# Optimization experiments

Measured on AMD Instinct MI355X. Metric: run time of the kernel, lower is better.

## Reference

```python
import jax, jax.numpy as jnp
import numpy as np

N_NODES = 100000
N_EDGES = 1600000
IN_CH = 128
HID = 128   # 2 * out_channels
OUT = 64


def setup_inputs() -> dict:
    key = jax.random.key(0)
    ks = jax.random.split(key, 5)
    x = jax.random.normal(ks[0], (N_NODES, IN_CH), dtype=jnp.float32)
    edge_index = jax.random.randint(ks[1], (2, N_EDGES), 0, N_NODES, dtype=jnp.int64)
    # Glorot-ish init for the two GCN weight matrices
    W1 = jax.random.normal(ks[2], (IN_CH, HID), dtype=jnp.float32) / np.sqrt(IN_CH)
    b1 = jnp.zeros((HID,), dtype=jnp.float32)
    W2 = jax.random.normal(ks[3], (HID, OUT), dtype=jnp.float32) / np.sqrt(HID)
    b2 = jnp.zeros((OUT,), dtype=jnp.float32)
    return {"x": x, "edge_index": edge_index, "W1": W1, "b1": b1, "W2": W2, "b2": b2}


def _gcn_conv(x, W, b, src, dst, coef, n):
    # Standard GCNConv: D^{-1/2} (A + I) D^{-1/2} X W + b
    xw = x @ W                                   # [N, F_out]
    msg = xw[src] * coef[:, None]                # gather + scale  [E+N, F_out]
    agg = jax.ops.segment_sum(msg, dst, num_segments=n)  # scatter-add [N, F_out]
    return agg + b


def reference(x, edge_index, W1, b1, W2, b2):
    n = x.shape[0]
    loops = jnp.arange(n, dtype=edge_index.dtype)
    src = jnp.concatenate([edge_index[0], loops])  # add self loops
    dst = jnp.concatenate([edge_index[1], loops])
    deg = jax.ops.segment_sum(jnp.ones_like(src, dtype=x.dtype), dst, num_segments=n)
    dinv = jnp.where(deg > 0, jax.lax.rsqrt(deg), 0.0)
    coef = dinv[src] * dinv[dst]                  # symmetric normalization per edge

    h = _gcn_conv(x, W1, b1, src, dst, coef, n)
    h = jax.nn.relu(h)                            # non_linearity=True
    # F.normalize(p=2, dim=-1) with eps clamp 1e-12; dropout inactive (eval mode)
    h = h / jnp.maximum(jnp.linalg.norm(h, axis=-1, keepdims=True), 1e-12)
    return _gcn_conv(h, W2, b2, src, dst, coef, n)
```

## Files before the change

### kernel.cpp

```cpp
#include <hip/hip_runtime.h>
#include <hip/hip_bf16.h>


#define IN_CH 128
#define HID 128
#define OUT_CH 64
#define NBLK 128
#define MAXNB 1568

typedef unsigned int uint_t;
typedef unsigned short ushort_t;
typedef __attribute__((ext_vector_type(8))) short bf16x8;
typedef __attribute__((ext_vector_type(4))) float f32x4;
typedef __attribute__((ext_vector_type(2))) float f32v2;

__device__ __forceinline__ ushort_t f32_to_bf16_rn(float f) {
    uint_t u = __float_as_uint(f);
    u = (u + 0x7fffu + ((u >> 16) & 1u)) >> 16;
    return (ushort_t)u;
}
__device__ __forceinline__ float bf16lo_to_f32(uint_t u) { return __uint_as_float(u << 16); }
__device__ __forceinline__ float bf16hi_to_f32(uint_t u) { return __uint_as_float(u & 0xffff0000u); }

__device__ __forceinline__ void acc_row(f32v2& a0, f32v2& a1, f32v2& a2, f32v2& a3,
                                        uint4 v) {
    a0 += (f32v2){bf16lo_to_f32(v.x), bf16hi_to_f32(v.x)};
    a1 += (f32v2){bf16lo_to_f32(v.y), bf16hi_to_f32(v.y)};
    a2 += (f32v2){bf16lo_to_f32(v.z), bf16hi_to_f32(v.z)};
    a3 += (f32v2){bf16lo_to_f32(v.w), bf16hi_to_f32(v.w)};
}
__device__ __forceinline__ void acc_row_c(f32v2& a0, f32v2& a1, f32v2& a2, f32v2& a3,
                                          uint4 v, float c) {
    f32v2 cv = {c, c};
    a0 += (f32v2){bf16lo_to_f32(v.x), bf16hi_to_f32(v.x)} * cv;
    a1 += (f32v2){bf16lo_to_f32(v.y), bf16hi_to_f32(v.y)} * cv;
    a2 += (f32v2){bf16lo_to_f32(v.z), bf16hi_to_f32(v.z)} * cv;
    a3 += (f32v2){bf16lo_to_f32(v.w), bf16hi_to_f32(v.w)} * cv;
}

__global__ __launch_bounds__(256) void hist_kernel(const int* __restrict__ dst, int E,
                                                   int chunk, int NB,
                                                   int* __restrict__ blk_cnt) {
    __shared__ int hist[MAXNB];
    int tid = threadIdx.x;
    int blk = blockIdx.x;
    for (int b = tid; b < NB; b += 256) hist[b] = 0;
    __syncthreads();
    int start = blk * chunk;
    int end = start + chunk; if (end > E) end = E;
    int e = start + tid;
    for (; e + 768 < end; e += 1024) {
        int d0 = dst[e], d1 = dst[e + 256], d2 = dst[e + 512], d3 = dst[e + 768];
        atomicAdd(&hist[d0 >> 6], 1);
        atomicAdd(&hist[d1 >> 6], 1);
        atomicAdd(&hist[d2 >> 6], 1);
        atomicAdd(&hist[d3 >> 6], 1);
    }
    for (; e < end; e += 256) atomicAdd(&hist[dst[e] >> 6], 1);
    __syncthreads();
    for (int b = tid; b < NB; b += 256) blk_cnt[blk * NB + b] = hist[b];
}

__global__ __launch_bounds__(256) void btot_kernel(const int* __restrict__ blk_cnt,
                                                   int NB, int* __restrict__ btot) {
    int b = blockIdx.x * 256 + threadIdx.x;
    if (b < NB) {
        int sum = 0;
        #pragma unroll 8
        for (int blk = 0; blk < NBLK; blk++) sum += blk_cnt[blk * NB + b];
        btot[b] = sum;
    }
}

__global__ __launch_bounds__(256) void scan_kernel(const int* __restrict__ btot, int NB,
                                                   int* __restrict__ bucket_base,
                                                   int* __restrict__ row_start,
                                                   int n, int E) {
    __shared__ int sdata[256];
    __shared__ int carryS;
    int tid = threadIdx.x;
    if (tid == 0) carryS = 0;
    __syncthreads();
    int nchunks = (NB + 255) / 256;
    for (int c = 0; c < nchunks; c++) {
        int i = c * 256 + tid;
        int v = (i < NB) ? btot[i] : 0;
        sdata[tid] = v;
        __syncthreads();
        for (int off = 1; off < 256; off <<= 1) {
            int t = (tid >= off) ? sdata[tid - off] : 0;
            __syncthreads();
            sdata[tid] += t;
            __syncthreads();
        }
        if (i < NB) bucket_base[i] = carryS + sdata[tid] - v;
        __syncthreads();
        if (tid == 0) carryS += sdata[255];
        __syncthreads();
    }
    if (tid == 0) {
        bucket_base[NB] = E;
        row_start[n] = E;
    }
}

__global__ __launch_bounds__(256) void colscan_kernel(const int* __restrict__ blk_cnt,
                                                      const int* __restrict__ bucket_base,
                                                      int NB, int* __restrict__ blk_start) {
    __shared__ int tile[NBLK][16];
    int tid = threadIdx.x;
    int b0 = blockIdx.x * 16;
    for (int idx = tid; idx < NBLK * 16; idx += 256) {
        int blk = idx >> 4, b = idx & 15;
        if (b0 + b < NB) tile[blk][b] = blk_cnt[blk * NB + b0 + b];
    }
    __syncthreads();
    if (tid < 16 && b0 + tid < NB) {
        int running = bucket_base[b0 + tid];
        for (int blk = 0; blk < NBLK; blk++) {
            int t = tile[blk][tid];
            tile[blk][tid] = running;
            running += t;
        }
    }
    __syncthreads();
    for (int idx = tid; idx < NBLK * 16; idx += 256) {
        int blk = idx >> 4, b = idx & 15;
        if (b0 + b < NB) blk_start[blk * NB + b0 + b] = tile[blk][b];
    }
}

__global__ __launch_bounds__(256) void scatter_kernel(const int* __restrict__ src,
                                                      const int* __restrict__ dst,
                                                      int E, int chunk, int NB,
                                                      const int* __restrict__ blk_start,
                                                      uint_t* __restrict__ pairs) {
    __shared__ int cur[MAXNB];
    int tid = threadIdx.x;
    int blk = blockIdx.x;
    for (int b = tid; b < NB; b += 256) cur[b] = blk_start[blk * NB + b];
    __syncthreads();
    int start = blk * chunk;
    int end = start + chunk; if (end > E) end = E;
    int e = start + tid;
    for (; e + 768 < end; e += 1024) {
        int d0 = dst[e], d1 = dst[e + 256], d2 = dst[e + 512], d3 = dst[e + 768];
        int s0 = src[e], s1 = src[e + 256], s2 = src[e + 512], s3 = src[e + 768];
        int p0 = atomicAdd(&cur[d0 >> 6], 1);
        int p1 = atomicAdd(&cur[d1 >> 6], 1);
        int p2 = atomicAdd(&cur[d2 >> 6], 1);
        int p3 = atomicAdd(&cur[d3 >> 6], 1);
        pairs[p0] = (uint_t)s0 | ((uint_t)(d0 & 63) << 26);
        pairs[p1] = (uint_t)s1 | ((uint_t)(d1 & 63) << 26);
        pairs[p2] = (uint_t)s2 | ((uint_t)(d2 & 63) << 26);
        pairs[p3] = (uint_t)s3 | ((uint_t)(d3 & 63) << 26);
    }
    for (; e < end; e += 256) {
        int d = dst[e], s = src[e];
        int p = atomicAdd(&cur[d >> 6], 1);
        pairs[p] = (uint_t)s | ((uint_t)(d & 63) << 26);
    }
}

__global__ __launch_bounds__(256) void fine_fill_kernel(const uint_t* __restrict__ pairs,
                                                        const int* __restrict__ bucket_base,
                                                        int* __restrict__ row_start,
                                                        float* __restrict__ dinv,
                                                        int* __restrict__ csr_src,
                                                        int n) {
    __shared__ int cnt64[64];
    __shared__ int cur[64];
    int b = blockIdx.x;
    int node0 = b << 6;
    int tid = threadIdx.x;
    if (tid < 64) cnt64[tid] = 0;
    __syncthreads();
    int start = bucket_base[b];
    int end = bucket_base[b + 1];
    int e = start + tid;
    for (; e + 768 < end; e += 1024) {
        uint_t u0 = pairs[e], u1 = pairs[e + 256], u2 = pairs[e + 512], u3 = pairs[e + 768];
        atomicAdd(&cnt64[u0 >> 26], 1);
        atomicAdd(&cnt64[u1 >> 26], 1);
        atomicAdd(&cnt64[u2 >> 26], 1);
        atomicAdd(&cnt64[u3 >> 26], 1);
    }
    for (; e < end; e += 256) atomicAdd(&cnt64[pairs[e] >> 26], 1);
    __syncthreads();
    if (tid < 64) {
        int c = cnt64[tid];
        int v = c;
        #pragma unroll
        for (int off = 1; off < 64; off <<= 1) {
            int u = __shfl_up(v, off, 64);
            if (tid >= off) v += u;
        }
        int excl = start + v - c;
        if (node0 + tid < n) {
            row_start[node0 + tid] = excl;
            dinv[node0 + tid] = rsqrtf((float)(c + 1));
        }
        cur[tid] = excl;
    }
    __syncthreads();
    e = start + tid;
    for (; e + 768 < end; e += 1024) {
        uint_t u0 = pairs[e], u1 = pairs[e + 256], u2 = pairs[e + 512], u3 = pairs[e + 768];
        int p0 = atomicAdd(&cur[u0 >> 26], 1);
        int p1 = atomicAdd(&cur[u1 >> 26], 1);
        int p2 = atomicAdd(&cur[u2 >> 26], 1);
        int p3 = atomicAdd(&cur[u3 >> 26], 1);
        csr_src[p0] = (int)(u0 & 0x3FFFFFFu);
        csr_src[p1] = (int)(u1 & 0x3FFFFFFu);
        csr_src[p2] = (int)(u2 & 0x3FFFFFFu);
        csr_src[p3] = (int)(u3 & 0x3FFFFFFu);
    }
    for (; e < end; e += 256) {
        uint_t u = pairs[e];
        int p = atomicAdd(&cur[u >> 26], 1);
        csr_src[p] = (int)(u & 0x3FFFFFFu);
    }
}

__global__ __launch_bounds__(256) void wsplit_kernel(const float* __restrict__ W1,
                                                     const float* __restrict__ W2,
                                                     ushort_t* __restrict__ w1h,
                                                     ushort_t* __restrict__ w1l,
                                                     ushort_t* __restrict__ w2h,
                                                     ushort_t* __restrict__ w2l) {
    int idx = blockIdx.x * 256 + threadIdx.x;
    const int tot1 = 128 * 128;
    const int tot = tot1 + 64 * 128;
    if (idx >= tot) return;
    float v;
    ushort_t* ph;
    ushort_t* pl;
    int o;
    if (idx < tot1) {
        int c = idx >> 7, k = idx & 127;
        v = W1[k * 128 + c];
        ph = w1h; pl = w1l; o = idx;
    } else {
        int j = idx - tot1;
        int c = j >> 7, k = j & 127;
        v = W2[k * 64 + c];
        ph = w2h; pl = w2l; o = j;
    }
    ushort_t h = f32_to_bf16_rn(v);
    float hv = __uint_as_float((uint_t)h << 16);
    ph[o] = h;
    pl[o] = f32_to_bf16_rn(v - hv);
}

template <int NCOL, bool F32_IN>
__global__ __launch_bounds__(256, 2) void mfma_gemm_kernel(const void* __restrict__ Xv,
                                                           const ushort_t* __restrict__ Wth,
                                                           const ushort_t* __restrict__ Wtl,
                                                           const float* __restrict__ rowscale,
                                                           ushort_t* __restrict__ Y, int n) {
    constexpr int NT = NCOL / 16;
    constexpr int WB = NCOL * 128 * 2;
    constexpr int NCH = WB / 16;
    __shared__ __align__(16) char Bs[2 * WB];

    int tid = threadIdx.x;

    for (int i = tid; i < 2 * NCH; i += 256) {
        bool lo = (i >= NCH);
        int j = lo ? i - NCH : i;
        int row = j >> 4, c = j & 15;
        bf16x8 v = *(const bf16x8*)((lo ? Wtl : Wth) + row * 128 + c * 8);
        int bo = (row << 8) + (c << 4);
        bo ^= (row & 7) << 4;
        *(bf16x8*)(Bs + (lo ? WB : 0) + bo) = v;
    }
    __syncthreads();

    int wave = tid >> 6;
    int lane = tid & 63;
    int q = lane >> 4;
    int r16 = lane & 15;
    int rowBase = blockIdx.x * 128 + wave * 32;
    int ar0 = rowBase + r16;      if (ar0 > n - 1) ar0 = n - 1;
    int ar1 = rowBase + 16 + r16; if (ar1 > n - 1) ar1 = n - 1;

    const float* X = (const float*)Xv;
    const ushort_t* Hb = (const ushort_t*)Xv;

    f32x4 acc[2][NT];
    #pragma unroll
    for (int rt = 0; rt < 2; rt++)
        #pragma unroll
        for (int t = 0; t < NT; t++) acc[rt][t] = (f32x4){0.f, 0.f, 0.f, 0.f};

    #pragma unroll
    for (int ks = 0; ks < 4; ks++) {
        int k0 = ks * 32 + q * 8;
        bf16x8 ah[2], al[2] = {};
        #pragma unroll
        for (int rt = 0; rt < 2; rt++) {
            int arow = rt ? ar1 : ar0;
            if (F32_IN) {
                const float4* xr = (const float4*)(X + (size_t)arow * 128 + k0);
                float4 p0 = xr[0], p1 = xr[1];
                float v[8] = {p0.x, p0.y, p0.z, p0.w, p1.x, p1.y, p1.z, p1.w};
                #pragma unroll
                for (int j = 0; j < 8; j++) {
                    ushort_t hb = f32_to_bf16_rn(v[j]);
                    float hv = __uint_as_float((uint_t)hb << 16);
                    ah[rt][j] = (short)hb;
                    al[rt][j] = (short)f32_to_bf16_rn(v[j] - hv);
                }
            } else {
                ah[rt] = *(const bf16x8*)(Hb + (size_t)arow * 128 + k0);
            }
        }
        #pragma unroll
        for (int t = 0; t < NT; t++) {
            int bo = ((t * 16 + r16) << 8) + ks * 64 + (q << 4);
            bo ^= (r16 & 7) << 4;
            bf16x8 bh = *(const bf16x8*)(Bs + bo);
            bf16x8 bl = *(const bf16x8*)(Bs + WB + bo);
            #pragma unroll
            for (int rt = 0; rt < 2; rt++) {
                acc[rt][t] = __builtin_amdgcn_mfma_f32_16x16x32_bf16(ah[rt], bh, acc[rt][t], 0, 0, 0);
                acc[rt][t] = __builtin_amdgcn_mfma_f32_16x16x32_bf16(ah[rt], bl, acc[rt][t], 0, 0, 0);
                if (F32_IN)
                    acc[rt][t] = __builtin_amdgcn_mfma_f32_16x16x32_bf16(al[rt], bh, acc[rt][t], 0, 0, 0);
            }
        }
    }

    #pragma unroll
    for (int rt = 0; rt < 2; rt++) {
        #pragma unroll
        for (int rr = 0; rr < 4; rr++) {
            int row = rowBase + rt * 16 + q * 4 + rr;
            if (row < n) {
                float rs = rowscale[row];
                #pragma unroll
                for (int t = 0; t < NT; t++)
                    Y[(size_t)row * NCOL + t * 16 + r16] = f32_to_bf16_rn(acc[rt][t][rr] * rs);
            }
        }
    }
}

__global__ __launch_bounds__(256) void agg1_kernel(const ushort_t* __restrict__ xw,
                                                   const int* __restrict__ csr_src,
                                                   const int* __restrict__ row_start,
                                                   const float* __restrict__ dinv,
                                                   const float* __restrict__ b1,
                                                   ushort_t* __restrict__ h, int n) {
    int wid = (blockIdx.x * 256 + threadIdx.x) >> 6;
    int lane = threadIdx.x & 63;
    if (wid >= n) return;
    int i = wid;
    int g = lane >> 4;
    int cb = lane & 15;
    const uint4* X4 = (const uint4*)xw;
    float di = dinv[i];
    int e0 = row_start[i], e1 = row_start[i + 1];

    f32v2 a0 = {0.f, 0.f}, a1 = {0.f, 0.f}, a2 = {0.f, 0.f}, a3 = {0.f, 0.f};
    {
        uint4 v = X4[(size_t)i * 16 + cb];
        acc_row_c(a0, a1, a2, a3, v, (g == 0) ? 1.0f : 0.0f);
    }
    int e = e0;
    for (; e + 16 <= e1; e += 16) {
        int s0 = csr_src[e + g];
        int s1 = csr_src[e + 4 + g];
        int s2 = csr_src[e + 8 + g];
        int s3 = csr_src[e + 12 + g];
        uint4 v0 = X4[(size_t)s0 * 16 + cb];
        uint4 v1 = X4[(size_t)s1 * 16 + cb];
        uint4 v2 = X4[(size_t)s2 * 16 + cb];
        uint4 v3 = X4[(size_t)s3 * 16 + cb];
        acc_row(a0, a1, a2, a3, v0);
        acc_row(a0, a1, a2, a3, v1);
        acc_row(a0, a1, a2, a3, v2);
        acc_row(a0, a1, a2, a3, v3);
    }
    if (e < e1) {
        int last = e1 - 1;
        int p0 = e + g, p1 = e + 4 + g, p2 = e + 8 + g, p3 = e + 12 + g;
        int s0 = csr_src[p0 <= last ? p0 : last];
        int s1 = csr_src[p1 <= last ? p1 : last];
        int s2 = csr_src[p2 <= last ? p2 : last];
        int s3 = csr_src[p3 <= last ? p3 : last];
        uint4 v0 = X4[(size_t)s0 * 16 + cb];
        uint4 v1 = X4[(size_t)s1 * 16 + cb];
        uint4 v2 = X4[(size_t)s2 * 16 + cb];
        uint4 v3 = X4[(size_t)s3 * 16 + cb];
        acc_row_c(a0, a1, a2, a3, v0, (p0 <= last) ? 1.0f : 0.0f);
        acc_row_c(a0, a1, a2, a3, v1, (p1 <= last) ? 1.0f : 0.0f);
        acc_row_c(a0, a1, a2, a3, v2, (p2 <= last) ? 1.0f : 0.0f);
        acc_row_c(a0, a1, a2, a3, v3, (p3 <= last) ? 1.0f : 0.0f);
    }
    #pragma unroll
    for (int m = 16; m <= 32; m <<= 1) {
        a0.x += __shfl_xor(a0.x, m, 64); a0.y += __shfl_xor(a0.y, m, 64);
        a1.x += __shfl_xor(a1.x, m, 64); a1.y += __shfl_xor(a1.y, m, 64);
        a2.x += __shfl_xor(a2.x, m, 64); a2.y += __shfl_xor(a2.y, m, 64);
        a3.x += __shfl_xor(a3.x, m, 64); a3.y += __shfl_xor(a3.y, m, 64);
    }
    const float2* bp = (const float2*)(b1 + cb * 8);
    float2 b0v = bp[0], b1v = bp[1], b2v = bp[2], b3v = bp[3];
    float vals[8];
    vals[0] = fmaxf(fmaf(a0.x, di, b0v.x), 0.f);
    vals[1] = fmaxf(fmaf(a0.y, di, b0v.y), 0.f);
    vals[2] = fmaxf(fmaf(a1.x, di, b1v.x), 0.f);
    vals[3] = fmaxf(fmaf(a1.y, di, b1v.y), 0.f);
    vals[4] = fmaxf(fmaf(a2.x, di, b2v.x), 0.f);
    vals[5] = fmaxf(fmaf(a2.y, di, b2v.y), 0.f);
    vals[6] = fmaxf(fmaf(a3.x, di, b3v.x), 0.f);
    vals[7] = fmaxf(fmaf(a3.y, di, b3v.y), 0.f);
    float ss = 0.f;
    #pragma unroll
    for (int j = 0; j < 8; j++) ss = fmaf(vals[j], vals[j], ss);
    #pragma unroll
    for (int m = 1; m <= 8; m <<= 1) ss += __shfl_xor(ss, m, 64);
    float scale = 1.0f / fmaxf(sqrtf(ss), 1e-12f);
    if (g == 0) {
        uint4 o;
        o.x = (uint_t)f32_to_bf16_rn(vals[0] * scale) | ((uint_t)f32_to_bf16_rn(vals[1] * scale) << 16);
        o.y = (uint_t)f32_to_bf16_rn(vals[2] * scale) | ((uint_t)f32_to_bf16_rn(vals[3] * scale) << 16);
        o.z = (uint_t)f32_to_bf16_rn(vals[4] * scale) | ((uint_t)f32_to_bf16_rn(vals[5] * scale) << 16);
        o.w = (uint_t)f32_to_bf16_rn(vals[6] * scale) | ((uint_t)f32_to_bf16_rn(vals[7] * scale) << 16);
        ((uint4*)h)[(size_t)i * 16 + cb] = o;
    }
}

__global__ __launch_bounds__(256) void agg2_kernel(const ushort_t* __restrict__ hw,
                                                   const int* __restrict__ csr_src,
                                                   const int* __restrict__ row_start,
                                                   const float* __restrict__ dinv,
                                                   const float* __restrict__ b2,
                                                   float* __restrict__ out, int n) {
    int wid = (blockIdx.x * 256 + threadIdx.x) >> 6;
    int lane = threadIdx.x & 63;
    int i = wid * 2 + (lane >> 5);
    int l = lane & 31;
    if (i >= n) return;
    float di = dinv[i];
    uint_t su = ((const uint_t*)(hw + (size_t)i * OUT_CH))[l];
    float ax = bf16lo_to_f32(su), ay = bf16hi_to_f32(su);
    int e0 = row_start[i], e1 = row_start[i + 1];
    int e = e0;
    for (; e + 8 <= e1; e += 8) {
        int s[8];
        #pragma unroll
        for (int j = 0; j < 8; j++) s[j] = csr_src[e + j];
        uint_t v[8];
        #pragma unroll
        for (int j = 0; j < 8; j++)
            v[j] = ((const uint_t*)(hw + (size_t)s[j] * OUT_CH))[l];
        #pragma unroll
        for (int j = 0; j < 8; j++) {
            ax += bf16lo_to_f32(v[j]);
            ay += bf16hi_to_f32(v[j]);
        }
    }
    if (e < e1) {
        int last = e1 - 1;
        int s[8];
        #pragma unroll
        for (int j = 0; j < 8; j++) {
            int idx = e + j;
            s[j] = csr_src[idx <= last ? idx : last];
        }
        uint_t v[8];
        #pragma unroll
        for (int j = 0; j < 8; j++)
            v[j] = ((const uint_t*)(hw + (size_t)s[j] * OUT_CH))[l];
        #pragma unroll
        for (int j = 0; j < 8; j++) {
            float c = (e + j <= last) ? 1.0f : 0.0f;
            ax = fmaf(bf16lo_to_f32(v[j]), c, ax);
            ay = fmaf(bf16hi_to_f32(v[j]), c, ay);
        }
    }
    ax = fmaf(ax, di, b2[l * 2]);
    ay = fmaf(ay, di, b2[l * 2 + 1]);
    ((float2*)(out + (size_t)i * OUT_CH))[l] = make_float2(ax, ay);
}

extern "C" void kernel_launch(void* const* d_in, const int* in_sizes, int n_in,
                              void* d_out, int out_size, void* d_ws, size_t ws_size,
                              hipStream_t stream) {
    const float* x  = (const float*)d_in[0];
    const int*   ei = (const int*)d_in[1];
    const float* W1 = (const float*)d_in[2];
    const float* b1 = (const float*)d_in[3];
    const float* W2 = (const float*)d_in[4];
    const float* b2 = (const float*)d_in[5];
    float* out = (float*)d_out;

    const int N = in_sizes[0] / IN_CH;
    const int E = in_sizes[1] / 2;
    const int* src = ei;
    const int* dst = ei + E;
    const int NB = (N + 63) / 64;
    const int chunk = (E + NBLK - 1) / NBLK;

    char* base = (char*)d_ws;
    size_t off = 0;
    auto alloc = [&](size_t bytes) -> void* {
        void* p = base + off;
        off = (off + bytes + 255) & ~(size_t)255;
        return p;
    };
    int*      blk_cnt     = (int*)alloc((size_t)NBLK * NB * 4);
    int*      blk_start   = (int*)alloc((size_t)NBLK * NB * 4);
    int*      btot        = (int*)alloc((size_t)NB * 4);
    int*      bucket_base = (int*)alloc((size_t)(NB + 1) * 4);
    int*      row_start   = (int*)alloc((size_t)(N + 1) * 4);
    float*    dinv        = (float*)alloc((size_t)N * 4);
    int*      csr_src     = (int*)alloc((size_t)E * 4);
    uint_t*   pairs       = (uint_t*)alloc((size_t)E * 4);
    ushort_t* xw          = (ushort_t*)alloc((size_t)N * HID * 2);
    ushort_t* h           = (ushort_t*)alloc((size_t)N * HID * 2);
    ushort_t* hw          = (ushort_t*)alloc((size_t)N * OUT_CH * 2);
    ushort_t* w1h         = (ushort_t*)alloc((size_t)128 * 128 * 2);
    ushort_t* w1l         = (ushort_t*)alloc((size_t)128 * 128 * 2);
    ushort_t* w2h         = (ushort_t*)alloc((size_t)64 * 128 * 2);
    ushort_t* w2l         = (ushort_t*)alloc((size_t)64 * 128 * 2);
    (void)ws_size;

    wsplit_kernel<<<(128 * 128 + 64 * 128 + 255) / 256, 256, 0, stream>>>(
        W1, W2, w1h, w1l, w2h, w2l);

    hist_kernel<<<NBLK, 256, 0, stream>>>(dst, E, chunk, NB, blk_cnt);
    btot_kernel<<<(NB + 255) / 256, 256, 0, stream>>>(blk_cnt, NB, btot);
    scan_kernel<<<1, 256, 0, stream>>>(btot, NB, bucket_base, row_start, N, E);
    colscan_kernel<<<(NB + 15) / 16, 256, 0, stream>>>(blk_cnt, bucket_base, NB, blk_start);
    scatter_kernel<<<NBLK, 256, 0, stream>>>(src, dst, E, chunk, NB, blk_start, pairs);
    fine_fill_kernel<<<NB, 256, 0, stream>>>(pairs, bucket_base, row_start, dinv,
                                             csr_src, N);

    mfma_gemm_kernel<128, true><<<(N + 127) / 128, 256, 0, stream>>>(
        x, w1h, w1l, dinv, xw, N);
    agg1_kernel<<<(N * 64 + 255) / 256, 256, 0, stream>>>(xw, csr_src, row_start,
                                                          dinv, b1, h, N);
    mfma_gemm_kernel<64, false><<<(N + 127) / 128, 256, 0, stream>>>(
        h, w2h, w2l, dinv, hw, N);
    int waves2 = (N + 1) / 2;
    agg2_kernel<<<(waves2 * 64 + 255) / 256, 256, 0, stream>>>(hw, csr_src, row_start,
                                                               dinv, b2, out, N);
}
```

Baseline: 293.0 us.

## Split layer-1 aggregation into two column-half passes with deferred normalization

Layer-1 aggregation now runs as two kernel launches, each gathering one 64-column half of the bf16 xw rows, so each pass touches a smaller working set that may fit better in cache. Because the L2 row norm now spans both halves, each pass writes unnormalized h plus a partial sum of squares. A small kernel combines the two partials into a per-row scale (dinv divided by the norm), which the second GEMM applies. The cost is gathering the CSR indices twice, two extra launches, and h being rounded to bf16 before normalization rather than after, which slightly changes precision.

```diff
diff --git a/kernel.cpp b/kernel.cpp
--- a/kernel.cpp
+++ b/kernel.cpp
@@ -346,66 +346,57 @@
     }
 }
 
-__global__ __launch_bounds__(256) void agg1_kernel(const ushort_t* __restrict__ xw,
-                                                   const int* __restrict__ csr_src,
-                                                   const int* __restrict__ row_start,
-                                                   const float* __restrict__ dinv,
-                                                   const float* __restrict__ b1,
-                                                   ushort_t* __restrict__ h, int n) {
+template <int HALF>
+__global__ __launch_bounds__(256) void agg1h_kernel(const ushort_t* __restrict__ xw,
+                                                    const int* __restrict__ csr_src,
+                                                    const int* __restrict__ row_start,
+                                                    const float* __restrict__ dinv,
+                                                    const float* __restrict__ b1,
+                                                    ushort_t* __restrict__ h,
+                                                    float* __restrict__ ssOut, int n) {
     int wid = (blockIdx.x * 256 + threadIdx.x) >> 6;
     int lane = threadIdx.x & 63;
     if (wid >= n) return;
     int i = wid;
-    int g = lane >> 4;
-    int cb = lane & 15;
+    int g = lane >> 3;
+    int cb = lane & 7;
     const uint4* X4 = (const uint4*)xw;
+    int hoff = HALF * 8 + cb;
     float di = dinv[i];
     int e0 = row_start[i], e1 = row_start[i + 1];
 
     f32v2 a0 = {0.f, 0.f}, a1 = {0.f, 0.f}, a2 = {0.f, 0.f}, a3 = {0.f, 0.f};
     {
-        uint4 v = X4[(size_t)i * 16 + cb];
+        uint4 v = X4[(size_t)i * 16 + hoff];
         acc_row_c(a0, a1, a2, a3, v, (g == 0) ? 1.0f : 0.0f);
     }
     int e = e0;
     for (; e + 16 <= e1; e += 16) {
         int s0 = csr_src[e + g];
-        int s1 = csr_src[e + 4 + g];
-        int s2 = csr_src[e + 8 + g];
-        int s3 = csr_src[e + 12 + g];
-        uint4 v0 = X4[(size_t)s0 * 16 + cb];
-        uint4 v1 = X4[(size_t)s1 * 16 + cb];
-        uint4 v2 = X4[(size_t)s2 * 16 + cb];
-        uint4 v3 = X4[(size_t)s3 * 16 + cb];
+        int s1 = csr_src[e + 8 + g];
+        uint4 v0 = X4[(size_t)s0 * 16 + hoff];
+        uint4 v1 = X4[(size_t)s1 * 16 + hoff];
         acc_row(a0, a1, a2, a3, v0);
         acc_row(a0, a1, a2, a3, v1);
-        acc_row(a0, a1, a2, a3, v2);
-        acc_row(a0, a1, a2, a3, v3);
     }
     if (e < e1) {
         int last = e1 - 1;
-        int p0 = e + g, p1 = e + 4 + g, p2 = e + 8 + g, p3 = e + 12 + g;
+        int p0 = e + g, p1 = e + 8 + g;
         int s0 = csr_src[p0 <= last ? p0 : last];
         int s1 = csr_src[p1 <= last ? p1 : last];
-        int s2 = csr_src[p2 <= last ? p2 : last];
-        int s3 = csr_src[p3 <= last ? p3 : last];
-        uint4 v0 = X4[(size_t)s0 * 16 + cb];
-        uint4 v1 = X4[(size_t)s1 * 16 + cb];
-        uint4 v2 = X4[(size_t)s2 * 16 + cb];
-        uint4 v3 = X4[(size_t)s3 * 16 + cb];
+        uint4 v0 = X4[(size_t)s0 * 16 + hoff];
+        uint4 v1 = X4[(size_t)s1 * 16 + hoff];
         acc_row_c(a0, a1, a2, a3, v0, (p0 <= last) ? 1.0f : 0.0f);
         acc_row_c(a0, a1, a2, a3, v1, (p1 <= last) ? 1.0f : 0.0f);
-        acc_row_c(a0, a1, a2, a3, v2, (p2 <= last) ? 1.0f : 0.0f);
-        acc_row_c(a0, a1, a2, a3, v3, (p3 <= last) ? 1.0f : 0.0f);
     }
     #pragma unroll
-    for (int m = 16; m <= 32; m <<= 1) {
+    for (int m = 8; m <= 32; m <<= 1) {
         a0.x += __shfl_xor(a0.x, m, 64); a0.y += __shfl_xor(a0.y, m, 64);
         a1.x += __shfl_xor(a1.x, m, 64); a1.y += __shfl_xor(a1.y, m, 64);
         a2.x += __shfl_xor(a2.x, m, 64); a2.y += __shfl_xor(a2.y, m, 64);
         a3.x += __shfl_xor(a3.x, m, 64); a3.y += __shfl_xor(a3.y, m, 64);
     }
-    const float2* bp = (const float2*)(b1 + cb * 8);
+    const float2* bp = (const float2*)(b1 + HALF * 64 + cb * 8);
     float2 b0v = bp[0], b1v = bp[1], b2v = bp[2], b3v = bp[3];
     float vals[8];
     vals[0] = fmaxf(fmaf(a0.x, di, b0v.x), 0.f);
@@ -420,15 +411,26 @@
     #pragma unroll
     for (int j = 0; j < 8; j++) ss = fmaf(vals[j], vals[j], ss);
     #pragma unroll
-    for (int m = 1; m <= 8; m <<= 1) ss += __shfl_xor(ss, m, 64);
-    float scale = 1.0f / fmaxf(sqrtf(ss), 1e-12f);
+    for (int m = 1; m <= 4; m <<= 1) ss += __shfl_xor(ss, m, 64);
+    if (lane == 0) ssOut[i] = ss;
     if (g == 0) {
         uint4 o;
-        o.x = (uint_t)f32_to_bf16_rn(vals[0] * scale) | ((uint_t)f32_to_bf16_rn(vals[1] * scale) << 16);
-        o.y = (uint_t)f32_to_bf16_rn(vals[2] * scale) | ((uint_t)f32_to_bf16_rn(vals[3] * scale) << 16);
-        o.z = (uint_t)f32_to_bf16_rn(vals[4] * scale) | ((uint_t)f32_to_bf16_rn(vals[5] * scale) << 16);
-        o.w = (uint_t)f32_to_bf16_rn(vals[6] * scale) | ((uint_t)f32_to_bf16_rn(vals[7] * scale) << 16);
-        ((uint4*)h)[(size_t)i * 16 + cb] = o;
+        o.x = (uint_t)f32_to_bf16_rn(vals[0]) | ((uint_t)f32_to_bf16_rn(vals[1]) << 16);
+        o.y = (uint_t)f32_to_bf16_rn(vals[2]) | ((uint_t)f32_to_bf16_rn(vals[3]) << 16);
+        o.z = (uint_t)f32_to_bf16_rn(vals[4]) | ((uint_t)f32_to_bf16_rn(vals[5]) << 16);
+        o.w = (uint_t)f32_to_bf16_rn(vals[6]) | ((uint_t)f32_to_bf16_rn(vals[7]) << 16);
+        ((uint4*)h)[(size_t)i * 16 + hoff] = o;
+    }
+}
+
+__global__ __launch_bounds__(256) void nrm_kernel(const float* __restrict__ ssA,
+                                                  const float* __restrict__ ssB,
+                                                  const float* __restrict__ dinv,
+                                                  float* __restrict__ rowscale2, int n) {
+    int i = blockIdx.x * 256 + threadIdx.x;
+    if (i < n) {
+        float norm = sqrtf(ssA[i] + ssB[i]);
+        rowscale2[i] = dinv[i] / fmaxf(norm, 1e-12f);
     }
 }
 
@@ -526,6 +528,9 @@
     ushort_t* w1l         = (ushort_t*)alloc((size_t)128 * 128 * 2);
     ushort_t* w2h         = (ushort_t*)alloc((size_t)64 * 128 * 2);
     ushort_t* w2l         = (ushort_t*)alloc((size_t)64 * 128 * 2);
+    float*    ssA         = (float*)alloc((size_t)N * 4);
+    float*    ssB         = (float*)alloc((size_t)N * 4);
+    float*    rowscale2   = (float*)alloc((size_t)N * 4);
     (void)ws_size;
 
     wsplit_kernel<<<(128 * 128 + 64 * 128 + 255) / 256, 256, 0, stream>>>(
@@ -541,10 +546,14 @@
 
     mfma_gemm_kernel<128, true><<<(N + 127) / 128, 256, 0, stream>>>(
         x, w1h, w1l, dinv, xw, N);
-    agg1_kernel<<<(N * 64 + 255) / 256, 256, 0, stream>>>(xw, csr_src, row_start,
-                                                          dinv, b1, h, N);
+    int aggGrid = (N * 64 + 255) / 256;
+    agg1h_kernel<0><<<aggGrid, 256, 0, stream>>>(xw, csr_src, row_start, dinv, b1,
+                                                 h, ssA, N);
+    agg1h_kernel<1><<<aggGrid, 256, 0, stream>>>(xw, csr_src, row_start, dinv, b1,
+                                                 h, ssB, N);
+    nrm_kernel<<<(N + 255) / 256, 256, 0, stream>>>(ssA, ssB, dinv, rowscale2, N);
     mfma_gemm_kernel<64, false><<<(N + 127) / 128, 256, 0, stream>>>(
-        h, w2h, w2l, dinv, hw, N);
+        h, w2h, w2l, rowscale2, hw, N);
     int waves2 = (N + 1) / 2;
     agg2_kernel<<<(waves2 * 64 + 255) / 256, 256, 0, stream>>>(hw, csr_src, row_start,
                                                                dinv, b2, out, N);
```

New measurement: 319.9 us. 9.2% more time.

## Restructure layer-2 aggregation to one wave per node with 8 edge groups

Applied to the files above, without the earlier changes.

Changes agg2 from two nodes per wave (32 lanes each loading 4 bytes per edge) to one node per wave where 8 lane groups each process a different edge with 16-byte vector loads, then combine partial sums via cross-lane shuffles. The aim is wider memory transactions and more independent gathers in flight per wave. The cost is twice as many waves, shuffle reduction overhead, and wasted lanes on low-degree nodes where the 32-edge tail path is masked.

```diff
diff --git a/kernel.cpp b/kernel.cpp
--- a/kernel.cpp
+++ b/kernel.cpp
@@ -440,50 +440,72 @@
                                                    float* __restrict__ out, int n) {
     int wid = (blockIdx.x * 256 + threadIdx.x) >> 6;
     int lane = threadIdx.x & 63;
-    int i = wid * 2 + (lane >> 5);
-    int l = lane & 31;
-    if (i >= n) return;
+    if (wid >= n) return;
+    int i = wid;
+    int g = lane >> 3;
+    int cb = lane & 7;
+    const uint4* H4 = (const uint4*)hw;
     float di = dinv[i];
-    uint_t su = ((const uint_t*)(hw + (size_t)i * OUT_CH))[l];
-    float ax = bf16lo_to_f32(su), ay = bf16hi_to_f32(su);
     int e0 = row_start[i], e1 = row_start[i + 1];
+
+    f32v2 a0 = {0.f, 0.f}, a1 = {0.f, 0.f}, a2 = {0.f, 0.f}, a3 = {0.f, 0.f};
+    {
+        uint4 v = H4[(size_t)i * 8 + cb];
+        acc_row_c(a0, a1, a2, a3, v, (g == 0) ? 1.0f : 0.0f);
+    }
     int e = e0;
-    for (; e + 8 <= e1; e += 8) {
-        int s[8];
-        #pragma unroll
-        for (int j = 0; j < 8; j++) s[j] = csr_src[e + j];
-        uint_t v[8];
-        #pragma unroll
-        for (int j = 0; j < 8; j++)
-            v[j] = ((const uint_t*)(hw + (size_t)s[j] * OUT_CH))[l];
-        #pragma unroll
-        for (int j = 0; j < 8; j++) {
-            ax += bf16lo_to_f32(v[j]);
-            ay += bf16hi_to_f32(v[j]);
-        }
+    for (; e + 32 <= e1; e += 32) {
+        int s0 = csr_src[e + g];
+        int s1 = csr_src[e + 8 + g];
+        int s2 = csr_src[e + 16 + g];
+        int s3 = csr_src[e + 24 + g];
+        uint4 v0 = H4[(size_t)s0 * 8 + cb];
+        uint4 v1 = H4[(size_t)s1 * 8 + cb];
+        uint4 v2 = H4[(size_t)s2 * 8 + cb];
+        uint4 v3 = H4[(size_t)s3 * 8 + cb];
+        acc_row(a0, a1, a2, a3, v0);
+        acc_row(a0, a1, a2, a3, v1);
+        acc_row(a0, a1, a2, a3, v2);
+        acc_row(a0, a1, a2, a3, v3);
     }
     if (e < e1) {
         int last = e1 - 1;
-        int s[8];
-        #pragma unroll
-        for (int j = 0; j < 8; j++) {
-            int idx = e + j;
-            s[j] = csr_src[idx <= last ? idx : last];
-        }
-        uint_t v[8];
-        #pragma unroll
-        for (int j = 0; j < 8; j++)
-            v[j] = ((const uint_t*)(hw + (size_t)s[j] * OUT_CH))[l];
-        #pragma unroll
-        for (int j = 0; j < 8; j++) {
-            float c = (e + j <= last) ? 1.0f : 0.0f;
-            ax = fmaf(bf16lo_to_f32(v[j]), c, ax);
-            ay = fmaf(bf16hi_to_f32(v[j]), c, ay);
-        }
-    }
-    ax = fmaf(ax, di, b2[l * 2]);
-    ay = fmaf(ay, di, b2[l * 2 + 1]);
-    ((float2*)(out + (size_t)i * OUT_CH))[l] = make_float2(ax, ay);
+        int p0 = e + g, p1 = e + 8 + g, p2 = e + 16 + g, p3 = e + 24 + g;
+        int s0 = csr_src[p0 <= last ? p0 : last];
+        int s1 = csr_src[p1 <= last ? p1 : last];
+        int s2 = csr_src[p2 <= last ? p2 : last];
+        int s3 = csr_src[p3 <= last ? p3 : last];
+        uint4 v0 = H4[(size_t)s0 * 8 + cb];
+        uint4 v1 = H4[(size_t)s1 * 8 + cb];
+        uint4 v2 = H4[(size_t)s2 * 8 + cb];
+        uint4 v3 = H4[(size_t)s3 * 8 + cb];
+        acc_row_c(a0, a1, a2, a3, v0, (p0 <= last) ? 1.0f : 0.0f);
+        acc_row_c(a0, a1, a2, a3, v1, (p1 <= last) ? 1.0f : 0.0f);
+        acc_row_c(a0, a1, a2, a3, v2, (p2 <= last) ? 1.0f : 0.0f);
+        acc_row_c(a0, a1, a2, a3, v3, (p3 <= last) ? 1.0f : 0.0f);
+    }
+    #pragma unroll
+    for (int m = 8; m <= 32; m <<= 1) {
+        a0.x += __shfl_xor(a0.x, m, 64); a0.y += __shfl_xor(a0.y, m, 64);
+        a1.x += __shfl_xor(a1.x, m, 64); a1.y += __shfl_xor(a1.y, m, 64);
+        a2.x += __shfl_xor(a2.x, m, 64); a2.y += __shfl_xor(a2.y, m, 64);
+        a3.x += __shfl_xor(a3.x, m, 64); a3.y += __shfl_xor(a3.y, m, 64);
+    }
+    if (g == 0) {
+        const float2* bp = (const float2*)(b2 + cb * 8);
+        float2 b0v = bp[0], b1v = bp[1], b2v = bp[2], b3v = bp[3];
+        float4 o0, o1;
+        o0.x = fmaf(a0.x, di, b0v.x);
+        o0.y = fmaf(a0.y, di, b0v.y);
+        o0.z = fmaf(a1.x, di, b1v.x);
+        o0.w = fmaf(a1.y, di, b1v.y);
+        o1.x = fmaf(a2.x, di, b2v.x);
+        o1.y = fmaf(a2.y, di, b2v.y);
+        o1.z = fmaf(a3.x, di, b3v.x);
+        o1.w = fmaf(a3.y, di, b3v.y);
+        ((float4*)out)[(size_t)i * 16 + cb * 2]     = o0;
+        ((float4*)out)[(size_t)i * 16 + cb * 2 + 1] = o1;
+    }
 }
 
 extern "C" void kernel_launch(void* const* d_in, const int* in_sizes, int n_in,
@@ -545,7 +567,6 @@
                                                           dinv, b1, h, N);
     mfma_gemm_kernel<64, false><<<(N + 127) / 128, 256, 0, stream>>>(
         h, w2h, w2l, dinv, hw, N);
-    int waves2 = (N + 1) / 2;
-    agg2_kernel<<<(waves2 * 64 + 255) / 256, 256, 0, stream>>>(hw, csr_src, row_start,
-                                                               dinv, b2, out, N);
-}
+    agg2_kernel<<<(N * 64 + 255) / 256, 256, 0, stream>>>(hw, csr_src, row_start,
+                                                          dinv, b2, out, N);
+}
```

Result: slower. 306.9 us (+4.8%).
